# Optimization experiments

Hardware: AMD Instinct MI355X
Metric: run time of the kernel (lower is better)

Reference implementation:

```python
import jax, jax.numpy as jnp
import numpy as np

B, L, D, H = 1024, 128, 768, 256
EPS = 1e-5  # torch BatchNorm1d default eps


def _masked_mean(x, lens):
    # x: [B, L, D], lens: [B] int -> mean over first lens[i] rows per sample
    mask = (jnp.arange(x.shape[1])[None, :] < lens[:, None]).astype(x.dtype)  # [B, L]
    return jnp.einsum('bld,bl->bd', x, mask) / lens[:, None].astype(x.dtype)


def _batchnorm_train(x, gamma, beta):
    # training-mode BN: batch mean and biased variance
    mu = jnp.mean(x, axis=0)
    var = jnp.mean((x - mu) ** 2, axis=0)
    return gamma * (x - mu) / jnp.sqrt(var + EPS) + beta


def setup_inputs() -> dict:
    key = jax.random.key(0)
    ks = jax.random.split(key, 12)
    user_features = jax.random.normal(ks[0], (B, L, D), jnp.float32)
    hashtag_features = jax.random.normal(ks[1], (B, L, D), jnp.float32)
    user_lens = jax.random.randint(ks[2], (B,), 1, L + 1, jnp.int32)
    hashtag_lens = jax.random.randint(ks[3], (B,), 1, L + 1, jnp.int32)
    def lin(k, fan_out, fan_in):
        bound = 1.0 / np.sqrt(fan_in)
        kw, kb = jax.random.split(k)
        w = jax.random.uniform(kw, (fan_out, fan_in), jnp.float32, -bound, bound)
        b = jax.random.uniform(kb, (fan_out,), jnp.float32, -bound, bound)
        return w, b
    fc1_w, fc1_b = lin(ks[4], D, 2 * D)
    fc2_w, fc2_b = lin(ks[5], H, D)
    fc3_w, fc3_b = lin(ks[6], 1, H)
    bn1_g = jnp.ones((D,), jnp.float32)
    bn1_b = jnp.zeros((D,), jnp.float32)
    bn2_g = jnp.ones((H,), jnp.float32)
    bn2_b = jnp.zeros((H,), jnp.float32)
    return {
        'user_features': user_features, 'hashtag_features': hashtag_features,
        'user_lens': user_lens, 'hashtag_lens': hashtag_lens,
        'fc1_w': fc1_w, 'fc1_b': fc1_b, 'bn1_g': bn1_g, 'bn1_b': bn1_b,
        'fc2_w': fc2_w, 'fc2_b': fc2_b, 'bn2_g': bn2_g, 'bn2_b': bn2_b,
        'fc3_w': fc3_w, 'fc3_b': fc3_b,
    }


def reference(user_features, hashtag_features, user_lens, hashtag_lens,
              fc1_w, fc1_b, bn1_g, bn1_b, fc2_w, fc2_b, bn2_g, bn2_b,
              fc3_w, fc3_b):
    # fused ragged mean pooling (replaces per-sample python loop)
    u = _masked_mean(user_features, user_lens)       # [B, D]
    h = _masked_mean(hashtag_features, hashtag_lens)  # [B, D]
    x = jnp.concatenate([u, h], axis=1)               # [B, 2D]
    x = jax.nn.relu(_batchnorm_train(x @ fc1_w.T + fc1_b, bn1_g, bn1_b))
    x = jax.nn.relu(_batchnorm_train(x @ fc2_w.T + fc2_b, bn2_g, bn2_b))
    out = jax.nn.sigmoid(x @ fc3_w.T + fc3_b)          # [B, 1]
    return out
```

## Files before the change

### kernel.cpp

```cpp
#include <hip/hip_runtime.h>
#include <cstdint>
#include <cstddef>

#define BATCH 1024
#define SEQL  128
#define DIM   768
#define HID   256
#define KIN1  1536
#define BN_EPS 1e-5f

typedef unsigned short u16;
typedef __attribute__((ext_vector_type(8))) short short8;
typedef __attribute__((ext_vector_type(4))) float f32x4;

__device__ __forceinline__ u16 f2bf(float f) {
  uint32_t u = __float_as_uint(f);
  return (u16)((u + 0x7fffu + ((u >> 16) & 1u)) >> 16);
}
__device__ __forceinline__ f32x4 ntl(const f32x4* p) { return __builtin_nontemporal_load(p); }
__device__ __forceinline__ float kred(float v) {
  v += __shfl_xor(v, 16);
  v += __shfl_xor(v, 32);
  return v;
}

#define PREP_BLK 168
#define POOL_BLK 2048
#define NW1Q (DIM * KIN1 / 4)
#define NW2Q (HID * DIM / 4)

__global__ __launch_bounds__(256) void pool_prep_kernel(
    const float* __restrict__ uf, const float* __restrict__ hf,
    const int* __restrict__ ul, const int* __restrict__ hl,
    const float* __restrict__ w1, const float* __restrict__ w2,
    u16* __restrict__ xb, u16* __restrict__ w1b, u16* __restrict__ w2b) {
  const int id = blockIdx.x;
  const int tid = threadIdx.x;
  if (id < PREP_BLK) {
    const int base = id * 256 + tid;
#pragma unroll
    for (int s = 0; s < 8; ++s) {
      const int i = base + s * (PREP_BLK * 256);
      if (i < NW1Q) {
        f32x4 v = ((const f32x4*)w1)[i];
        ((ushort4*)w1b)[i] = make_ushort4(f2bf(v[0]), f2bf(v[1]), f2bf(v[2]), f2bf(v[3]));
      } else {
        const int i2 = i - NW1Q;
        if (i2 < NW2Q) {
          f32x4 v = ((const f32x4*)w2)[i2];
          ((ushort4*)w2b)[i2] = make_ushort4(f2bf(v[0]), f2bf(v[1]), f2bf(v[2]), f2bf(v[3]));
        }
      }
    }
    return;
  }
  __shared__ f32x4 sacc[4][192];
  const int pj = id - PREP_BLK;
  const int b = pj >> 1;
  const int which = pj & 1;
  const f32x4* src = (const f32x4*)((which ? hf : uf) + (size_t)b * (SEQL * DIM));
  const int len = which ? hl[b] : ul[b];
  const int wave = tid >> 6, lane = tid & 63;

  const int nrows = (len > wave) ? (((len - 1 - wave) >> 2) + 1) : 0;
  const f32x4* base = src + (size_t)wave * 192 + lane;

  f32x4 a0 = (f32x4){0.f, 0.f, 0.f, 0.f}, a1 = a0, a2 = a0;
  f32x4 b0 = a0, b1 = a0, b2 = a0;

  if (nrows >= 2) {
    const f32x4* p = base;
    const f32x4* q = base + 768;
    f32x4 c0 = ntl(p), c1 = ntl(p + 64), c2 = ntl(p + 128);
    f32x4 c3 = ntl(q), c4 = ntl(q + 64), c5 = ntl(q + 128);
    int i = 2;
    for (; i + 1 < nrows; i += 2) {
      const f32x4* pn = base + (size_t)i * 768;
      const f32x4* qn = pn + 768;
      f32x4 n0 = ntl(pn), n1 = ntl(pn + 64), n2 = ntl(pn + 128);
      f32x4 n3 = ntl(qn), n4 = ntl(qn + 64), n5 = ntl(qn + 128);
      a0 += c0; a1 += c1; a2 += c2;
      b0 += c3; b1 += c4; b2 += c5;
      c0 = n0; c1 = n1; c2 = n2; c3 = n3; c4 = n4; c5 = n5;
    }
    a0 += c0; a1 += c1; a2 += c2;
    b0 += c3; b1 += c4; b2 += c5;
  }
  if (nrows & 1) {
    const f32x4* p = base + (size_t)(nrows - 1) * 768;
    a0 += ntl(p); a1 += ntl(p + 64); a2 += ntl(p + 128);
  }
  a0 += b0; a1 += b1; a2 += b2;

  sacc[wave][lane] = a0;
  sacc[wave][64 + lane] = a1;
  sacc[wave][128 + lane] = a2;
  __syncthreads();
  if (tid < 192) {
    f32x4 t = sacc[0][tid] + sacc[1][tid] + sacc[2][tid] + sacc[3][tid];
    const float s = 1.f / (float)len;
    ushort4 o = make_ushort4(f2bf(t[0] * s), f2bf(t[1] * s), f2bf(t[2] * s), f2bf(t[3] * s));
    *(ushort4*)(xb + (size_t)b * KIN1 + which * DIM + tid * 4) = o;
  }
}

#define LDT 72

__global__ __launch_bounds__(256) void gemm1_kernel(
    const u16* __restrict__ A, const u16* __restrict__ W,
    const float* __restrict__ bias, float* __restrict__ y, float* __restrict__ p1) {
  __shared__ u16 lA[2][64 * LDT];
  __shared__ u16 lB[2][64 * LDT];
  __shared__ float red[2][64][2];
  const int K = KIN1, N = DIM;
  const int tid = threadIdx.x, lane = tid & 63, wv = tid >> 6;
  const int wr = wv >> 1, wc = wv & 1;
  const int r16 = lane & 15, kgrp = lane >> 4;
  const int d = blockIdx.x;
  const int g = d & 7, j = d >> 3;
  const int bm = (g >> 1) * 4 + (j & 3);
  const int bn = (g & 1) * 6 + (j >> 2);
  const int sr = tid >> 3, sc8 = (tid & 7) * 8;

  f32x4 acc[2][2];
#pragma unroll
  for (int mi = 0; mi < 2; ++mi)
#pragma unroll
    for (int ni = 0; ni < 2; ++ni) acc[mi][ni] = (f32x4){0.f, 0.f, 0.f, 0.f};

  const u16* Ab = A + (size_t)bm * 64 * K;
  const u16* Wb = W + (size_t)bn * 64 * K;

  uint4 ra0, ra1, rb0, rb1;
#define G1_LOAD(k0)                                              \
  ra0 = *(const uint4*)(Ab + (size_t)sr * K + (k0) + sc8);       \
  ra1 = *(const uint4*)(Ab + (size_t)(sr + 32) * K + (k0) + sc8);\
  rb0 = *(const uint4*)(Wb + (size_t)sr * K + (k0) + sc8);       \
  rb1 = *(const uint4*)(Wb + (size_t)(sr + 32) * K + (k0) + sc8);
#define G1_WRITE(buf)                                \
  *(uint4*)(lA[buf] + sr * LDT + sc8) = ra0;         \
  *(uint4*)(lA[buf] + (sr + 32) * LDT + sc8) = ra1;  \
  *(uint4*)(lB[buf] + sr * LDT + sc8) = rb0;         \
  *(uint4*)(lB[buf] + (sr + 32) * LDT + sc8) = rb1;

  G1_LOAD(0)
  G1_WRITE(0)
  __syncthreads();
  const int nk = K / 64;
  for (int ti = 0; ti < nk; ++ti) {
    const int cur = ti & 1;
    const bool more = (ti + 1 < nk);
    if (more) { G1_LOAD((ti + 1) * 64) }
#pragma unroll
    for (int kk = 0; kk < 2; ++kk) {
      const int koff = (kk * 4 + kgrp) * 8;
      short8 af0 = *(const short8*)(lA[cur] + (wr * 32 + r16) * LDT + koff);
      short8 af1 = *(const short8*)(lA[cur] + (wr * 32 + 16 + r16) * LDT + koff);
      short8 bf0 = *(const short8*)(lB[cur] + (wc * 32 + r16) * LDT + koff);
      short8 bf1 = *(const short8*)(lB[cur] + (wc * 32 + 16 + r16) * LDT + koff);
      acc[0][0] = __builtin_amdgcn_mfma_f32_16x16x32_bf16(af0, bf0, acc[0][0], 0, 0, 0);
      acc[0][1] = __builtin_amdgcn_mfma_f32_16x16x32_bf16(af0, bf1, acc[0][1], 0, 0, 0);
      acc[1][0] = __builtin_amdgcn_mfma_f32_16x16x32_bf16(af1, bf0, acc[1][0], 0, 0, 0);
      acc[1][1] = __builtin_amdgcn_mfma_f32_16x16x32_bf16(af1, bf1, acc[1][1], 0, 0, 0);
    }
    if (more) { G1_WRITE(cur ^ 1) }
    __syncthreads();
  }
#undef G1_LOAD
#undef G1_WRITE

#pragma unroll
  for (int ni = 0; ni < 2; ++ni) {
    const int col = bn * 64 + wc * 32 + ni * 16 + r16;
    const float bv = bias[col];
    float s = 0.f, s2 = 0.f;
#pragma unroll
    for (int mi = 0; mi < 2; ++mi)
#pragma unroll
      for (int rg = 0; rg < 4; ++rg) {
        const int row = bm * 64 + wr * 32 + mi * 16 + kgrp * 4 + rg;
        const float v = acc[mi][ni][rg] + bv;
        y[(size_t)row * N + col] = v;
        s += v; s2 += v * v;
      }
    s = kred(s); s2 = kred(s2);
    if (lane < 16) {
      red[wr][wc * 32 + ni * 16 + r16][0] = s;
      red[wr][wc * 32 + ni * 16 + r16][1] = s2;
    }
  }
  __syncthreads();
  if (tid < 128) {
    const int col = tid >> 1, wh = tid & 1;
    p1[((size_t)bm * DIM + bn * 64 + col) * 2 + wh] = red[0][col][wh] + red[1][col][wh];
  }
}

__global__ __launch_bounds__(256) void gemm2_kernel(
    const float* __restrict__ y1, const u16* __restrict__ W,
    const float* __restrict__ bias, const float* __restrict__ g, const float* __restrict__ be,
    const float* __restrict__ p1, float* __restrict__ y2, float* __restrict__ p2) {
  __shared__ u16 lA[2][32 * LDT];
  __shared__ u16 lB[2][32 * LDT];
  __shared__ float sS[DIM], sH[DIM];
  __shared__ float red[2][32][2];
  const int K = DIM, N = HID;
  const int tid = threadIdx.x, lane = tid & 63, wv = tid >> 6;
  const int wr = wv >> 1, wc = wv & 1;
  const int r16 = lane & 15, kgrp = lane >> 4;
  const int d = blockIdx.x;
  const int g8 = d & 7, j = d >> 3;
  const int bm = g8 * 4 + (j & 3);
  const int bn = j >> 2;
  const int sr = tid >> 3, sc8 = (tid & 7) * 8;

  for (int c = tid; c < DIM; c += 256) {
    float s = 0.f, s2 = 0.f;
#pragma unroll
    for (int i = 0; i < 16; ++i) {
      float2 pv = *(const float2*)(p1 + ((size_t)i * DIM + c) * 2);
      s += pv.x; s2 += pv.y;
    }
    const float m = s * (1.f / BATCH);
    const float var = s2 * (1.f / BATCH) - m * m;
    const float r = rsqrtf(var + BN_EPS);
    const float scl = r * g[c];
    sS[c] = scl;
    sH[c] = be[c] - m * scl;
  }
  __syncthreads();

  f32x4 acc = (f32x4){0.f, 0.f, 0.f, 0.f};
  const float* Ab = y1 + (size_t)bm * 32 * K;
  const u16* Wb = W + (size_t)bn * 32 * K;

  f32x4 va0, va1;
  uint4 rbq;
#define G2_LOAD(k0)                                          \
  va0 = *(const f32x4*)(Ab + (size_t)sr * K + (k0) + sc8);   \
  va1 = *(const f32x4*)(Ab + (size_t)sr * K + (k0) + sc8 + 4);\
  rbq = *(const uint4*)(Wb + (size_t)sr * K + (k0) + sc8);

  auto pack_write = [&](int buf, int k0) {
    union { ushort us[8]; uint4 q; } pk;
#pragma unroll
    for (int jj = 0; jj < 4; ++jj) {
      pk.us[jj]     = f2bf(fmaxf(0.f, va0[jj] * sS[k0 + sc8 + jj] + sH[k0 + sc8 + jj]));
      pk.us[4 + jj] = f2bf(fmaxf(0.f, va1[jj] * sS[k0 + sc8 + 4 + jj] + sH[k0 + sc8 + 4 + jj]));
    }
    *(uint4*)(lA[buf] + sr * LDT + sc8) = pk.q;
    *(uint4*)(lB[buf] + sr * LDT + sc8) = rbq;
  };

  G2_LOAD(0)
  pack_write(0, 0);
  __syncthreads();
  const int nk = K / 64;
  for (int ti = 0; ti < nk; ++ti) {
    const int cur = ti & 1;
    const bool more = (ti + 1 < nk);
    if (more) { G2_LOAD((ti + 1) * 64) }
#pragma unroll
    for (int kk = 0; kk < 2; ++kk) {
      const int koff = (kk * 4 + kgrp) * 8;
      short8 af0 = *(const short8*)(lA[cur] + (wr * 16 + r16) * LDT + koff);
      short8 bf0 = *(const short8*)(lB[cur] + (wc * 16 + r16) * LDT + koff);
      acc = __builtin_amdgcn_mfma_f32_16x16x32_bf16(af0, bf0, acc, 0, 0, 0);
    }
    if (more) pack_write(cur ^ 1, (ti + 1) * 64);
    __syncthreads();
  }
#undef G2_LOAD

  {
    const int col = bn * 32 + wc * 16 + r16;
    const float bv = bias[col];
    float s = 0.f, s2 = 0.f;
#pragma unroll
    for (int rg = 0; rg < 4; ++rg) {
      const int row = bm * 32 + wr * 16 + kgrp * 4 + rg;
      const float v = acc[rg] + bv;
      y2[(size_t)row * N + col] = v;
      s += v; s2 += v * v;
    }
    s = kred(s); s2 = kred(s2);
    if (lane < 16) {
      red[wr][wc * 16 + r16][0] = s;
      red[wr][wc * 16 + r16][1] = s2;
    }
  }
  __syncthreads();
  if (tid < 64) {
    const int col = tid >> 1, wh = tid & 1;
    p2[((size_t)bm * HID + bn * 32 + col) * 2 + wh] = red[0][col][wh] + red[1][col][wh];
  }
}

__global__ __launch_bounds__(256) void fc3_kernel(
    const float* __restrict__ y2, const float* __restrict__ p2,
    const float* __restrict__ g, const float* __restrict__ be,
    const float* __restrict__ w3, const float* __restrict__ b3, float* __restrict__ out) {
  __shared__ float sS[HID], sH[HID];
  const int tid = threadIdx.x;
  {
    const int c = tid;
    float s = 0.f, s2 = 0.f;
#pragma unroll
    for (int i = 0; i < 32; ++i) {
      float2 pv = *(const float2*)(p2 + ((size_t)i * HID + c) * 2);
      s += pv.x; s2 += pv.y;
    }
    const float m = s * (1.f / BATCH);
    const float var = s2 * (1.f / BATCH) - m * m;
    const float r = rsqrtf(var + BN_EPS);
    const float scl = r * g[c];
    sS[c] = scl;
    sH[c] = be[c] - m * scl;
  }
  __syncthreads();
  const int row = blockIdx.x * 4 + (tid >> 6);
  const int lane = tid & 63;
  f32x4 xv = *(const f32x4*)(y2 + (size_t)row * HID + lane * 4);
  f32x4 sc = *(const f32x4*)&sS[lane * 4];
  f32x4 sh = *(const f32x4*)&sH[lane * 4];
  f32x4 wv = *(const f32x4*)(w3 + lane * 4);
  float dsum = 0.f;
#pragma unroll
  for (int jj = 0; jj < 4; ++jj) dsum += fmaxf(0.f, xv[jj] * sc[jj] + sh[jj]) * wv[jj];
#pragma unroll
  for (int off = 32; off > 0; off >>= 1) dsum += __shfl_xor(dsum, off);
  if (lane == 0) out[row] = 1.f / (1.f + expf(-(dsum + b3[0])));
}

extern "C" void kernel_launch(void* const* d_in, const int* in_sizes, int n_in,
                              void* d_out, int out_size, void* d_ws, size_t ws_size,
                              hipStream_t stream) {
  const float* uf   = (const float*)d_in[0];
  const float* hf   = (const float*)d_in[1];
  const int*   ul   = (const int*)d_in[2];
  const int*   hl   = (const int*)d_in[3];
  const float* fc1w = (const float*)d_in[4];
  const float* fc1b = (const float*)d_in[5];
  const float* bn1g = (const float*)d_in[6];
  const float* bn1b = (const float*)d_in[7];
  const float* fc2w = (const float*)d_in[8];
  const float* fc2b = (const float*)d_in[9];
  const float* bn2g = (const float*)d_in[10];
  const float* bn2b = (const float*)d_in[11];
  const float* fc3w = (const float*)d_in[12];
  const float* fc3b = (const float*)d_in[13];
  float* out = (float*)d_out;

  char* ws = (char*)d_ws;
  u16*   xb  = (u16*)  (ws + 0);
  u16*   w1b = (u16*)  (ws + 3145728);
  u16*   w2b = (u16*)  (ws + 5505024);
  float* y1  = (float*)(ws + 5898240);
  float* y2  = (float*)(ws + 9043968);
  float* p1  = (float*)(ws + 10092544);
  float* p2  = (float*)(ws + 10190848);

  pool_prep_kernel<<<PREP_BLK + POOL_BLK, 256, 0, stream>>>(uf, hf, ul, hl, fc1w, fc2w, xb, w1b, w2b);
  gemm1_kernel<<<192, 256, 0, stream>>>(xb, w1b, fc1b, y1, p1);
  gemm2_kernel<<<256, 256, 0, stream>>>(y1, w2b, fc2b, bn1g, bn1b, p1, y2, p2);
  fc3_kernel<<<256, 256, 0, stream>>>(y2, p2, bn2g, bn2b, fc3w, fc3b, out);
}
```

Measured before the change: 112.9 us.

## Split ragged pooling into two sequence chunks with a combine kernel

Each (sample, feature) pooling job is split into two 64-row chunks handled by separate blocks. Partial sums go to a float workspace that aliases y1, and a new combine kernel adds them, scales by 1/len and writes bf16. The goal is better load balance and more blocks in flight across the ragged lengths, at the cost of an extra launch and a partial-sum round trip. Nontemporal loads are also replaced with ordinary loads.

Measured after the change: 137.7 us. 21.9% more time.

```diff
diff --git a/kernel.cpp b/kernel.cpp
--- a/kernel.cpp
+++ b/kernel.cpp
@@ -17,7 +17,6 @@
   uint32_t u = __float_as_uint(f);
   return (u16)((u + 0x7fffu + ((u >> 16) & 1u)) >> 16);
 }
-__device__ __forceinline__ f32x4 ntl(const f32x4* p) { return __builtin_nontemporal_load(p); }
 __device__ __forceinline__ float kred(float v) {
   v += __shfl_xor(v, 16);
   v += __shfl_xor(v, 32);
@@ -25,15 +24,15 @@
 }
 
 #define PREP_BLK 168
-#define POOL_BLK 2048
+#define NCHUNK_BLK 4096
 #define NW1Q (DIM * KIN1 / 4)
 #define NW2Q (HID * DIM / 4)
 
-__global__ __launch_bounds__(256) void pool_prep_kernel(
+__global__ __launch_bounds__(256) void pool_partial_kernel(
     const float* __restrict__ uf, const float* __restrict__ hf,
     const int* __restrict__ ul, const int* __restrict__ hl,
     const float* __restrict__ w1, const float* __restrict__ w2,
-    u16* __restrict__ xb, u16* __restrict__ w1b, u16* __restrict__ w2b) {
+    float* __restrict__ part, u16* __restrict__ w1b, u16* __restrict__ w2b) {
   const int id = blockIdx.x;
   const int tid = threadIdx.x;
   if (id < PREP_BLK) {
@@ -54,41 +53,37 @@
     }
     return;
   }
+  const int pj = id - PREP_BLK;
+  const int c = pj & 1;
+  const int j = pj >> 1;
+  const int b = j >> 1;
+  const int which = j & 1;
+  const int len = which ? hl[b] : ul[b];
+  const int lo = c * 64;
+  if (len <= lo) return;
+  const int hi = (len < lo + 64) ? len : (lo + 64);
+
   __shared__ f32x4 sacc[4][192];
-  const int pj = id - PREP_BLK;
-  const int b = pj >> 1;
-  const int which = pj & 1;
+  const int wave = tid >> 6, lane = tid & 63;
   const f32x4* src = (const f32x4*)((which ? hf : uf) + (size_t)b * (SEQL * DIM));
-  const int len = which ? hl[b] : ul[b];
-  const int wave = tid >> 6, lane = tid & 63;
-
-  const int nrows = (len > wave) ? (((len - 1 - wave) >> 2) + 1) : 0;
-  const f32x4* base = src + (size_t)wave * 192 + lane;
 
   f32x4 a0 = (f32x4){0.f, 0.f, 0.f, 0.f}, a1 = a0, a2 = a0;
   f32x4 b0 = a0, b1 = a0, b2 = a0;
-
-  if (nrows >= 2) {
-    const f32x4* p = base;
-    const f32x4* q = base + 768;
-    f32x4 c0 = ntl(p), c1 = ntl(p + 64), c2 = ntl(p + 128);
-    f32x4 c3 = ntl(q), c4 = ntl(q + 64), c5 = ntl(q + 128);
-    int i = 2;
-    for (; i + 1 < nrows; i += 2) {
-      const f32x4* pn = base + (size_t)i * 768;
-      const f32x4* qn = pn + 768;
-      f32x4 n0 = ntl(pn), n1 = ntl(pn + 64), n2 = ntl(pn + 128);
-      f32x4 n3 = ntl(qn), n4 = ntl(qn + 64), n5 = ntl(qn + 128);
-      a0 += c0; a1 += c1; a2 += c2;
-      b0 += c3; b1 += c4; b2 += c5;
-      c0 = n0; c1 = n1; c2 = n2; c3 = n3; c4 = n4; c5 = n5;
-    }
-    a0 += c0; a1 += c1; a2 += c2;
-    b0 += c3; b1 += c4; b2 += c5;
-  }
-  if (nrows & 1) {
-    const f32x4* p = base + (size_t)(nrows - 1) * 768;
-    a0 += ntl(p); a1 += ntl(p + 64); a2 += ntl(p + 128);
+  int l = lo + wave;
+  for (; l + 4 < hi; l += 8) {
+    f32x4 v0 = src[(size_t)l * 192 + lane];
+    f32x4 v1 = src[(size_t)l * 192 + 64 + lane];
+    f32x4 v2 = src[(size_t)l * 192 + 128 + lane];
+    f32x4 u0 = src[(size_t)(l + 4) * 192 + lane];
+    f32x4 u1 = src[(size_t)(l + 4) * 192 + 64 + lane];
+    f32x4 u2 = src[(size_t)(l + 4) * 192 + 128 + lane];
+    a0 += v0; a1 += v1; a2 += v2;
+    b0 += u0; b1 += u1; b2 += u2;
+  }
+  if (l < hi) {
+    a0 += src[(size_t)l * 192 + lane];
+    a1 += src[(size_t)l * 192 + 64 + lane];
+    a2 += src[(size_t)l * 192 + 128 + lane];
   }
   a0 += b0; a1 += b1; a2 += b2;
 
@@ -98,10 +93,24 @@
   __syncthreads();
   if (tid < 192) {
     f32x4 t = sacc[0][tid] + sacc[1][tid] + sacc[2][tid] + sacc[3][tid];
-    const float s = 1.f / (float)len;
-    ushort4 o = make_ushort4(f2bf(t[0] * s), f2bf(t[1] * s), f2bf(t[2] * s), f2bf(t[3] * s));
-    *(ushort4*)(xb + (size_t)b * KIN1 + which * DIM + tid * 4) = o;
-  }
+    ((f32x4*)part)[(size_t)pj * 192 + tid] = t;
+  }
+}
+
+__global__ __launch_bounds__(192) void pool_combine_kernel(
+    const int* __restrict__ ul, const int* __restrict__ hl,
+    const float* __restrict__ part, u16* __restrict__ xb) {
+  const int j = blockIdx.x;
+  const int b = j >> 1;
+  const int which = j & 1;
+  const int len = which ? hl[b] : ul[b];
+  const int tid = threadIdx.x;
+  const f32x4* base = (const f32x4*)part + (size_t)j * 384;
+  f32x4 t = base[tid];
+  if (len > 64) t += base[192 + tid];
+  const float s = 1.f / (float)len;
+  ushort4 o = make_ushort4(f2bf(t[0] * s), f2bf(t[1] * s), f2bf(t[2] * s), f2bf(t[3] * s));
+  *(ushort4*)(xb + (size_t)b * KIN1 + which * DIM + tid * 4) = o;
 }
 
 #define LDT 72
@@ -352,15 +361,18 @@
   float* out = (float*)d_out;
 
   char* ws = (char*)d_ws;
-  u16*   xb  = (u16*)  (ws + 0);
-  u16*   w1b = (u16*)  (ws + 3145728);
-  u16*   w2b = (u16*)  (ws + 5505024);
-  float* y1  = (float*)(ws + 5898240);
-  float* y2  = (float*)(ws + 9043968);
-  float* p1  = (float*)(ws + 10092544);
-  float* p2  = (float*)(ws + 10190848);
-
-  pool_prep_kernel<<<PREP_BLK + POOL_BLK, 256, 0, stream>>>(uf, hf, ul, hl, fc1w, fc2w, xb, w1b, w2b);
+  u16*   xb   = (u16*)  (ws + 0);
+  u16*   w1b  = (u16*)  (ws + 3145728);
+  u16*   w2b  = (u16*)  (ws + 5505024);
+  float* part = (float*)(ws + 5898240);
+  float* y1   = (float*)(ws + 5898240);
+  float* y2   = (float*)(ws + 9043968);
+  float* p1   = (float*)(ws + 10092544);
+  float* p2   = (float*)(ws + 10190848);
+
+  pool_partial_kernel<<<PREP_BLK + NCHUNK_BLK, 256, 0, stream>>>(
+      uf, hf, ul, hl, fc1w, fc2w, part, w1b, w2b);
+  pool_combine_kernel<<<2048, 192, 0, stream>>>(ul, hl, part, xb);
   gemm1_kernel<<<192, 256, 0, stream>>>(xb, w1b, fc1b, y1, p1);
   gemm2_kernel<<<256, 256, 0, stream>>>(y1, w2b, fc2b, bn1g, bn1b, p1, y2, p2);
   fc3_kernel<<<256, 256, 0, stream>>>(y2, p2, bn2g, bn2b, fc3w, fc3b, out);
```
